# Kernel optimization log

Measured on AMD Instinct MI355X. Metric: run time of the kernel, lower is better.

Reference implementation:

```python
import jax, jax.numpy as jnp
import numpy as np

N_TOTAL = 204800  # total valid nodes across the batch
B = 1024          # number of graphs
D = 512           # input_dim (dim_node)
H = 512           # hidden width of NonLinearClassifier
C = 52            # num_classes
EPS = 1e-5        # BatchNorm eps


def setup_inputs() -> dict:
    key = jax.random.key(0)
    kz, k1, k2, k3 = jax.random.split(key, 4)
    # ragged per-graph node counts summing exactly to N_TOTAL
    rng = np.random.default_rng(0)
    counts = rng.integers(50, 350, size=B).astype(np.float64)
    counts = np.floor(counts * N_TOTAL / counts.sum()).astype(np.int64)
    counts[-1] += N_TOTAL - counts.sum()
    assert counts.min() > 0 and counts.sum() == N_TOTAL
    return {
        "z": jax.random.normal(kz, (N_TOTAL, D), dtype=jnp.float32),
        "batch_num_nodes": jnp.asarray(counts, dtype=jnp.int64),
        "w1": jax.random.normal(k1, (D, H), dtype=jnp.float32) * 0.02,
        "b1": jnp.zeros((H,), jnp.float32),
        "g1": jnp.ones((H,), jnp.float32),
        "beta1": jnp.zeros((H,), jnp.float32),
        "w2": jax.random.normal(k2, (H, H), dtype=jnp.float32) * 0.02,
        "b2": jnp.zeros((H,), jnp.float32),
        "g2": jnp.ones((H,), jnp.float32),
        "beta2": jnp.zeros((H,), jnp.float32),
        "w3": jax.random.normal(k3, (H, C), dtype=jnp.float32) * 0.02,
        "b3": jnp.zeros((C,), jnp.float32),
    }


def _batchnorm(x, gamma, beta):
    # training-mode BatchNorm1d: batch statistics (biased variance)
    m = x.mean(axis=0)
    v = x.var(axis=0)
    return gamma * (x - m) * jax.lax.rsqrt(v + EPS) + beta


def reference(z, batch_num_nodes, w1, b1, g1, beta1, w2, b2, g2, beta2, w3, b3):
    # fused segment-mean pooling (replaces torch.split + per-graph .mean loop)
    seg_ids = jnp.repeat(jnp.arange(B), batch_num_nodes, total_repeat_length=N_TOTAL)
    sums = jax.ops.segment_sum(z, seg_ids, num_segments=B)          # [B, D]
    graph_feats = sums / batch_num_nodes.astype(z.dtype)[:, None]   # [B, D]
    # NonLinearClassifier MLP (dropout inactive in eval / deterministic ref)
    h = jax.nn.relu(_batchnorm(graph_feats @ w1 + b1, g1, beta1))
    h = jax.nn.relu(_batchnorm(h @ w2 + b2, g2, beta2))
    return h @ w3 + b3  # [B, C] logits
```

## Files before the change

### kernel.cpp

```cpp
#include <hip/hip_runtime.h>

#define N_TOTAL 204800
#define NB 1024
#define DIM 512
#define NC 52
#define BN_EPS 1e-5f

__device__ inline void f4add(float4& a, const float4 b) {
    a.x += b.x; a.y += b.y; a.z += b.z; a.w += b.w;
}

__device__ inline float bn_relu1(float v, int f,
                                 const float* __restrict__ s1, const float* __restrict__ s2,
                                 const float* __restrict__ g, const float* __restrict__ beta) {
    float m  = s1[f] * (1.0f / NB);
    float vv = s2[f] * (1.0f / NB) - m * m;
    float is = rsqrtf(vv + BN_EPS);
    float h  = g[f] * (v - m) * is + beta[f];
    return h > 0.f ? h : 0.f;
}

__global__ __launch_bounds__(1024) void k_scan(const int* __restrict__ bnn,
                                               int* __restrict__ offs,
                                               int* __restrict__ cnt,
                                               float* __restrict__ inv,
                                               float* __restrict__ stats ) {
    __shared__ int red[1024];
    int tid = threadIdx.x;
    int v32 = bnn[tid];
    red[tid] = v32;
    __syncthreads();
    for (int s = 512; s > 0; s >>= 1) {
        if (tid < s) red[tid] += red[tid + s];
        __syncthreads();
    }
    int total = red[0];
    __syncthreads();
    int c = (total == N_TOTAL) ? v32 : bnn[2 * tid];
    red[tid] = c;
    __syncthreads();
    for (int off = 1; off < 1024; off <<= 1) {
        int t = (tid >= off) ? red[tid - off] : 0;
        __syncthreads();
        red[tid] += t;
        __syncthreads();
    }
    offs[tid] = red[tid] - c;
    cnt[tid]  = c;
    inv[tid]  = 1.0f / (float)c;
    stats[tid]        = 0.0f;
    stats[tid + 1024] = 0.0f;
}

__global__ __launch_bounds__(256) void k_pool(const float* __restrict__ z,
                                              const int* __restrict__ offs,
                                              const int* __restrict__ cnt,
                                              const float* __restrict__ inv,
                                              float* __restrict__ X) {
    __shared__ float4 buf[128];
    int g = blockIdx.x;
    int s0 = offs[g];
    int n  = cnt[g];
    float r = inv[g];
    int c4 = threadIdx.x & 127;
    int rp = threadIdx.x >> 7;
    const float4* p = (const float4*)z + (size_t)s0 * 128 + c4;
    float4 a0 = {0,0,0,0}, a1 = {0,0,0,0}, a2 = {0,0,0,0}, a3 = {0,0,0,0};
    int i = rp;
    for (; i + 6 < n; i += 8) {
        float4 v0 = p[(size_t)(i + 0) * 128];
        float4 v1 = p[(size_t)(i + 2) * 128];
        float4 v2 = p[(size_t)(i + 4) * 128];
        float4 v3 = p[(size_t)(i + 6) * 128];
        f4add(a0, v0); f4add(a1, v1); f4add(a2, v2); f4add(a3, v3);
    }
    for (; i < n; i += 2) { float4 v = p[(size_t)i * 128]; f4add(a0, v); }
    f4add(a0, a1); f4add(a2, a3); f4add(a0, a2);
    if (rp == 1) buf[c4] = a0;
    __syncthreads();
    if (rp == 0) {
        f4add(a0, buf[c4]);
        a0.x *= r; a0.y *= r; a0.z *= r; a0.w *= r;
        ((float4*)X)[(size_t)g * 128 + c4] = a0;
    }
}

template <bool BNA>
__global__ __launch_bounds__(256) void k_gemm64(const float* __restrict__ A,
                                                const float* __restrict__ W,
                                                const float* __restrict__ bias,
                                                const float* __restrict__ ps1,
                                                const float* __restrict__ ps2,
                                                const float* __restrict__ gam,
                                                const float* __restrict__ bet,
                                                float* __restrict__ Y,
                                                float* __restrict__ os1,
                                                float* __restrict__ os2) {
    __shared__ float As[32][68];
    __shared__ float Ws[32][68];
    int tid = threadIdx.x;
    int tx = tid & 15, ty = tid >> 4;
    int gr0 = blockIdx.x * 64;
    int gc0 = blockIdx.y * 64;
    float acc[4][4] = {};

    for (int k0 = 0; k0 < DIM; k0 += 32) {
#pragma unroll
        for (int it = 0; it < 2; it++) {
            int idx = it * 256 + tid;
            int row = idx >> 3;
            int kq  = idx & 7;
            int f0  = k0 + kq * 4;
            float4 v = *(const float4*)&A[(size_t)(gr0 + row) * DIM + f0];
            if (BNA) {
                v.x = bn_relu1(v.x, f0 + 0, ps1, ps2, gam, bet);
                v.y = bn_relu1(v.y, f0 + 1, ps1, ps2, gam, bet);
                v.z = bn_relu1(v.z, f0 + 2, ps1, ps2, gam, bet);
                v.w = bn_relu1(v.w, f0 + 3, ps1, ps2, gam, bet);
            }
            As[kq * 4 + 0][row] = v.x;
            As[kq * 4 + 1][row] = v.y;
            As[kq * 4 + 2][row] = v.z;
            As[kq * 4 + 3][row] = v.w;
        }
#pragma unroll
        for (int it = 0; it < 2; it++) {
            int idx = it * 256 + tid;
            int k  = idx >> 4;
            int cq = idx & 15;
            *(float4*)&Ws[k][cq * 4] =
                *(const float4*)&W[(size_t)(k0 + k) * DIM + gc0 + cq * 4];
        }
        __syncthreads();
#pragma unroll
        for (int k = 0; k < 32; k++) {
            float4 a = *(const float4*)&As[k][ty * 4];
            float4 w = *(const float4*)&Ws[k][tx * 4];
            acc[0][0] += a.x * w.x; acc[0][1] += a.x * w.y; acc[0][2] += a.x * w.z; acc[0][3] += a.x * w.w;
            acc[1][0] += a.y * w.x; acc[1][1] += a.y * w.y; acc[1][2] += a.y * w.z; acc[1][3] += a.y * w.w;
            acc[2][0] += a.z * w.x; acc[2][1] += a.z * w.y; acc[2][2] += a.z * w.z; acc[2][3] += a.z * w.w;
            acc[3][0] += a.w * w.x; acc[3][1] += a.w * w.y; acc[3][2] += a.w * w.z; acc[3][3] += a.w * w.w;
        }
        __syncthreads();
    }

    float4 b = *(const float4*)&bias[gc0 + tx * 4];
    float s[4] = {}, q[4] = {};
#pragma unroll
    for (int i = 0; i < 4; i++) {
        float4 y;
        y.x = acc[i][0] + b.x;
        y.y = acc[i][1] + b.y;
        y.z = acc[i][2] + b.z;
        y.w = acc[i][3] + b.w;
        *(float4*)&Y[(size_t)(gr0 + ty * 4 + i) * DIM + gc0 + tx * 4] = y;
        s[0] += y.x; q[0] += y.x * y.x;
        s[1] += y.y; q[1] += y.y * y.y;
        s[2] += y.z; q[2] += y.z * y.z;
        s[3] += y.w; q[3] += y.w * y.w;
    }
#pragma unroll
    for (int j = 0; j < 4; j++) {
        atomicAdd(&os1[gc0 + tx * 4 + j], s[j]);
        atomicAdd(&os2[gc0 + tx * 4 + j], q[j]);
    }
}

__global__ __launch_bounds__(256) void k_gemm3(const float* __restrict__ Y2,
                                               const float* __restrict__ W,
                                               const float* __restrict__ bias,
                                               const float* __restrict__ s1,
                                               const float* __restrict__ s2,
                                               const float* __restrict__ gam,
                                               const float* __restrict__ bet,
                                               float* __restrict__ out) {
    __shared__ float As[4][DIM];
    int tid = threadIdx.x;
    int r0 = blockIdx.x * 4;
#pragma unroll
    for (int it = 0; it < 2; it++) {
        int idx = it * 256 + tid;
        int row = idx >> 7;
        int cq  = idx & 127;
        int f   = cq * 4;
        float4 v = *(const float4*)&Y2[(size_t)(r0 + row) * DIM + f];
        v.x = bn_relu1(v.x, f + 0, s1, s2, gam, bet);
        v.y = bn_relu1(v.y, f + 1, s1, s2, gam, bet);
        v.z = bn_relu1(v.z, f + 2, s1, s2, gam, bet);
        v.w = bn_relu1(v.w, f + 3, s1, s2, gam, bet);
        *(float4*)&As[row][f] = v;
    }
    __syncthreads();
    int col = tid & 63;
    int row = tid >> 6;
    if (col < NC) {
        float acc = 0.f;
#pragma unroll 8
        for (int k = 0; k < DIM; k += 4) {
            float4 a = *(const float4*)&As[row][k];
            acc += a.x * W[(size_t)(k + 0) * NC + col];
            acc += a.y * W[(size_t)(k + 1) * NC + col];
            acc += a.z * W[(size_t)(k + 2) * NC + col];
            acc += a.w * W[(size_t)(k + 3) * NC + col];
        }
        out[(size_t)(r0 + row) * NC + col] = acc + bias[col];
    }
}

extern "C" void kernel_launch(void* const* d_in, const int* in_sizes, int n_in,
                              void* d_out, int out_size, void* d_ws, size_t ws_size,
                              hipStream_t stream) {
    const float* z   = (const float*)d_in[0];
    const int*   bnn = (const int*)d_in[1];
    const float* w1  = (const float*)d_in[2];
    const float* b1  = (const float*)d_in[3];
    const float* g1  = (const float*)d_in[4];
    const float* be1 = (const float*)d_in[5];
    const float* w2  = (const float*)d_in[6];
    const float* b2  = (const float*)d_in[7];
    const float* g2  = (const float*)d_in[8];
    const float* be2 = (const float*)d_in[9];
    const float* w3  = (const float*)d_in[10];
    const float* b3  = (const float*)d_in[11];

    int*   offs  = (int*)d_ws;
    int*   cnt   = offs + 1024;
    float* inv   = (float*)(cnt + 1024);
    float* stats = inv + 1024;
    float* X     = stats + 2048;
    float* Y1    = X  + (size_t)NB * DIM;
    float* Y2    = Y1 + (size_t)NB * DIM;
    float* out   = (float*)d_out;

    k_scan<<<1, 1024, 0, stream>>>(bnn, offs, cnt, inv, stats);
    k_pool<<<NB, 256, 0, stream>>>(z, offs, cnt, inv, X);

    dim3 gg(NB / 64, DIM / 64);
    k_gemm64<false><<<gg, 256, 0, stream>>>(X, w1, b1,
                                            nullptr, nullptr, nullptr, nullptr,
                                            Y1, stats, stats + 512);
    k_gemm64<true><<<gg, 256, 0, stream>>>(Y1, w2, b2,
                                           stats, stats + 512, g1, be1,
                                           Y2, stats + 1024, stats + 1536);
    k_gemm3<<<NB / 4, 256, 0, stream>>>(Y2, w3, b3,
                                        stats + 1024, stats + 1536, g2, be2, out);
}
```

Baseline: 711.9 us.

## Shrink GEMM tiles to 32x64, prefetch next K-tile, reduce BN stats via shuffles

The two hidden-layer GEMMs now use 32x64 output tiles instead of 64x64, which doubles the block count to fill more CUs. They also register-prefetch the next K slice of A and W while computing on the current one. The per-column BN sum and sum-of-squares are pre-reduced across rows with wave shuffles so only a quarter of threads issue atomics. The pooling loop is unrolled to 16 rows per iteration for more loads in flight. In exchange, each tile reuses less data and registers per thread go up.

```diff
diff --git a/kernel.cpp b/kernel.cpp
--- a/kernel.cpp
+++ b/kernel.cpp
@@ -67,12 +67,17 @@
     const float4* p = (const float4*)z + (size_t)s0 * 128 + c4;
     float4 a0 = {0,0,0,0}, a1 = {0,0,0,0}, a2 = {0,0,0,0}, a3 = {0,0,0,0};
     int i = rp;
-    for (; i + 6 < n; i += 8) {
+    for (; i + 14 < n; i += 16) {
         float4 v0 = p[(size_t)(i + 0) * 128];
         float4 v1 = p[(size_t)(i + 2) * 128];
         float4 v2 = p[(size_t)(i + 4) * 128];
         float4 v3 = p[(size_t)(i + 6) * 128];
+        float4 v4 = p[(size_t)(i + 8) * 128];
+        float4 v5 = p[(size_t)(i + 10) * 128];
+        float4 v6 = p[(size_t)(i + 12) * 128];
+        float4 v7 = p[(size_t)(i + 14) * 128];
         f4add(a0, v0); f4add(a1, v1); f4add(a2, v2); f4add(a3, v3);
+        f4add(a0, v4); f4add(a1, v5); f4add(a2, v6); f4add(a3, v7);
     }
     for (; i < n; i += 2) { float4 v = p[(size_t)i * 128]; f4add(a0, v); }
     f4add(a0, a1); f4add(a2, a3); f4add(a0, a2);
@@ -86,60 +91,66 @@
 }
 
 template <bool BNA>
-__global__ __launch_bounds__(256) void k_gemm64(const float* __restrict__ A,
-                                                const float* __restrict__ W,
-                                                const float* __restrict__ bias,
-                                                const float* __restrict__ ps1,
-                                                const float* __restrict__ ps2,
-                                                const float* __restrict__ gam,
-                                                const float* __restrict__ bet,
-                                                float* __restrict__ Y,
-                                                float* __restrict__ os1,
-                                                float* __restrict__ os2) {
-    __shared__ float As[32][68];
+__global__ __launch_bounds__(256) void k_gemm32x64(const float* __restrict__ A,
+                                                   const float* __restrict__ W,
+                                                   const float* __restrict__ bias,
+                                                   const float* __restrict__ ps1,
+                                                   const float* __restrict__ ps2,
+                                                   const float* __restrict__ gam,
+                                                   const float* __restrict__ bet,
+                                                   float* __restrict__ Y,
+                                                   float* __restrict__ os1,
+                                                   float* __restrict__ os2) {
+    __shared__ float As[32][34];
     __shared__ float Ws[32][68];
     int tid = threadIdx.x;
     int tx = tid & 15, ty = tid >> 4;
-    int gr0 = blockIdx.x * 64;
+    int gr0 = blockIdx.x * 32;
     int gc0 = blockIdx.y * 64;
-    float acc[4][4] = {};
-
-    for (int k0 = 0; k0 < DIM; k0 += 32) {
-#pragma unroll
-        for (int it = 0; it < 2; it++) {
-            int idx = it * 256 + tid;
-            int row = idx >> 3;
-            int kq  = idx & 7;
-            int f0  = k0 + kq * 4;
-            float4 v = *(const float4*)&A[(size_t)(gr0 + row) * DIM + f0];
-            if (BNA) {
-                v.x = bn_relu1(v.x, f0 + 0, ps1, ps2, gam, bet);
-                v.y = bn_relu1(v.y, f0 + 1, ps1, ps2, gam, bet);
-                v.z = bn_relu1(v.z, f0 + 2, ps1, ps2, gam, bet);
-                v.w = bn_relu1(v.w, f0 + 3, ps1, ps2, gam, bet);
-            }
-            As[kq * 4 + 0][row] = v.x;
-            As[kq * 4 + 1][row] = v.y;
-            As[kq * 4 + 2][row] = v.z;
-            As[kq * 4 + 3][row] = v.w;
-        }
-#pragma unroll
-        for (int it = 0; it < 2; it++) {
-            int idx = it * 256 + tid;
-            int k  = idx >> 4;
-            int cq = idx & 15;
-            *(float4*)&Ws[k][cq * 4] =
-                *(const float4*)&W[(size_t)(k0 + k) * DIM + gc0 + cq * 4];
-        }
-        __syncthreads();
+
+    int arow = tid >> 3;
+    int akq  = tid & 7;
+    int wk0 = tid >> 4;
+    int wcq = tid & 15;
+
+    float acc[2][4] = {};
+
+    float4 ra  = *(const float4*)&A[(size_t)(gr0 + arow) * DIM + akq * 4];
+    float4 rw0 = *(const float4*)&W[(size_t)wk0 * DIM + gc0 + wcq * 4];
+    float4 rw1 = *(const float4*)&W[(size_t)(wk0 + 16) * DIM + gc0 + wcq * 4];
+
+    for (int kt = 0; kt < 16; kt++) {
+        float4 v = ra;
+        if (BNA) {
+            int f0 = kt * 32 + akq * 4;
+            v.x = bn_relu1(v.x, f0 + 0, ps1, ps2, gam, bet);
+            v.y = bn_relu1(v.y, f0 + 1, ps1, ps2, gam, bet);
+            v.z = bn_relu1(v.z, f0 + 2, ps1, ps2, gam, bet);
+            v.w = bn_relu1(v.w, f0 + 3, ps1, ps2, gam, bet);
+        }
+        As[akq * 4 + 0][arow] = v.x;
+        As[akq * 4 + 1][arow] = v.y;
+        As[akq * 4 + 2][arow] = v.z;
+        As[akq * 4 + 3][arow] = v.w;
+        *(float4*)&Ws[wk0][wcq * 4]      = rw0;
+        *(float4*)&Ws[wk0 + 16][wcq * 4] = rw1;
+        __syncthreads();
+
+        if (kt < 15) {
+            int k0 = (kt + 1) * 32;
+            ra  = *(const float4*)&A[(size_t)(gr0 + arow) * DIM + k0 + akq * 4];
+            rw0 = *(const float4*)&W[(size_t)(k0 + wk0) * DIM + gc0 + wcq * 4];
+            rw1 = *(const float4*)&W[(size_t)(k0 + wk0 + 16) * DIM + gc0 + wcq * 4];
+        }
+
 #pragma unroll
         for (int k = 0; k < 32; k++) {
-            float4 a = *(const float4*)&As[k][ty * 4];
+            float2 a = *(const float2*)&As[k][ty * 2];
             float4 w = *(const float4*)&Ws[k][tx * 4];
-            acc[0][0] += a.x * w.x; acc[0][1] += a.x * w.y; acc[0][2] += a.x * w.z; acc[0][3] += a.x * w.w;
-            acc[1][0] += a.y * w.x; acc[1][1] += a.y * w.y; acc[1][2] += a.y * w.z; acc[1][3] += a.y * w.w;
-            acc[2][0] += a.z * w.x; acc[2][1] += a.z * w.y; acc[2][2] += a.z * w.z; acc[2][3] += a.z * w.w;
-            acc[3][0] += a.w * w.x; acc[3][1] += a.w * w.y; acc[3][2] += a.w * w.z; acc[3][3] += a.w * w.w;
+            acc[0][0] += a.x * w.x; acc[0][1] += a.x * w.y;
+            acc[0][2] += a.x * w.z; acc[0][3] += a.x * w.w;
+            acc[1][0] += a.y * w.x; acc[1][1] += a.y * w.y;
+            acc[1][2] += a.y * w.z; acc[1][3] += a.y * w.w;
         }
         __syncthreads();
     }
@@ -147,13 +158,13 @@
     float4 b = *(const float4*)&bias[gc0 + tx * 4];
     float s[4] = {}, q[4] = {};
 #pragma unroll
-    for (int i = 0; i < 4; i++) {
+    for (int i = 0; i < 2; i++) {
         float4 y;
         y.x = acc[i][0] + b.x;
         y.y = acc[i][1] + b.y;
         y.z = acc[i][2] + b.z;
         y.w = acc[i][3] + b.w;
-        *(float4*)&Y[(size_t)(gr0 + ty * 4 + i) * DIM + gc0 + tx * 4] = y;
+        *(float4*)&Y[(size_t)(gr0 + ty * 2 + i) * DIM + gc0 + tx * 4] = y;
         s[0] += y.x; q[0] += y.x * y.x;
         s[1] += y.y; q[1] += y.y * y.y;
         s[2] += y.z; q[2] += y.z * y.z;
@@ -161,8 +172,15 @@
     }
 #pragma unroll
     for (int j = 0; j < 4; j++) {
-        atomicAdd(&os1[gc0 + tx * 4 + j], s[j]);
-        atomicAdd(&os2[gc0 + tx * 4 + j], q[j]);
+        s[j] += __shfl_xor(s[j], 16); s[j] += __shfl_xor(s[j], 32);
+        q[j] += __shfl_xor(q[j], 16); q[j] += __shfl_xor(q[j], 32);
+    }
+    if ((ty & 3) == 0) {
+#pragma unroll
+        for (int j = 0; j < 4; j++) {
+            atomicAdd(&os1[gc0 + tx * 4 + j], s[j]);
+            atomicAdd(&os2[gc0 + tx * 4 + j], q[j]);
+        }
     }
 }
 
@@ -235,13 +253,13 @@
     k_scan<<<1, 1024, 0, stream>>>(bnn, offs, cnt, inv, stats);
     k_pool<<<NB, 256, 0, stream>>>(z, offs, cnt, inv, X);
 
-    dim3 gg(NB / 64, DIM / 64);
-    k_gemm64<false><<<gg, 256, 0, stream>>>(X, w1, b1,
-                                            nullptr, nullptr, nullptr, nullptr,
-                                            Y1, stats, stats + 512);
-    k_gemm64<true><<<gg, 256, 0, stream>>>(Y1, w2, b2,
-                                           stats, stats + 512, g1, be1,
-                                           Y2, stats + 1024, stats + 1536);
+    dim3 gg(NB / 32, DIM / 64);
+    k_gemm32x64<false><<<gg, 256, 0, stream>>>(X, w1, b1,
+                                               nullptr, nullptr, nullptr, nullptr,
+                                               Y1, stats, stats + 512);
+    k_gemm32x64<true><<<gg, 256, 0, stream>>>(Y1, w2, b2,
+                                              stats, stats + 512, g1, be1,
+                                              Y2, stats + 1024, stats + 1536);
     k_gemm3<<<NB / 4, 256, 0, stream>>>(Y2, w3, b3,
                                         stats + 1024, stats + 1536, g2, be2, out);
 }
```

Measured after the change: 658.1 us. 7.6% less time.
